# Optimization experiments

Hardware: AMD Instinct MI355X
Metric: run time of the kernel (lower is better)

The kernel has to match this reference:

```python
import jax, jax.numpy as jnp
import numpy as np

N_NODES = 50000
N_EDGES = 640000
F_IN = 64
EDGE_DIM = 16
HID = 128
N_LAYERS = 3
N_CLASSES = 2
NUM_GRAPHS = 64
BN_EPS = 1e-5


def setup_inputs() -> dict:
    key = jax.random.key(0)
    ks = jax.random.split(key, 20)
    s = 0.05
    inp = {
        "x": jax.random.normal(ks[0], (N_NODES, F_IN), dtype=jnp.float32),
        "edge_index": jax.random.randint(ks[1], (2, N_EDGES), 0, N_NODES, dtype=jnp.int32),
        "edge_attr": jax.random.normal(ks[2], (N_EDGES, EDGE_DIM), dtype=jnp.float32),
        "batch": jnp.sort(jax.random.randint(ks[3], (N_NODES,), 0, NUM_GRAPHS, dtype=jnp.int32)),
        # node encoder
        "enc_W": jax.random.normal(ks[4], (F_IN, HID), dtype=jnp.float32) * s,
        "enc_b": jnp.zeros((HID,), dtype=jnp.float32),
        # per-layer GINEConv params (stacked over layers)
        "edge_W": jax.random.normal(ks[5], (N_LAYERS, EDGE_DIM, HID), dtype=jnp.float32) * s,
        "edge_b": jnp.zeros((N_LAYERS, HID), dtype=jnp.float32),
        "mlp_W1": jax.random.normal(ks[6], (N_LAYERS, HID, HID), dtype=jnp.float32) * s,
        "mlp_b1": jnp.zeros((N_LAYERS, HID), dtype=jnp.float32),
        "mlp_W2": jax.random.normal(ks[7], (N_LAYERS, HID, HID), dtype=jnp.float32) * s,
        "mlp_b2": jnp.zeros((N_LAYERS, HID), dtype=jnp.float32),
        "bn_gamma": jnp.ones((N_LAYERS, HID), dtype=jnp.float32),
        "bn_beta": jnp.zeros((N_LAYERS, HID), dtype=jnp.float32),
        # classification head
        "head_W1": jax.random.normal(ks[8], (HID, HID), dtype=jnp.float32) * s,
        "head_b1": jnp.zeros((HID,), dtype=jnp.float32),
        "head_W2": jax.random.normal(ks[9], (HID, N_CLASSES), dtype=jnp.float32) * s,
        "head_b2": jnp.zeros((N_CLASSES,), dtype=jnp.float32),
    }
    return inp


def reference(x, edge_index, edge_attr, batch, enc_W, enc_b, edge_W, edge_b,
              mlp_W1, mlp_b1, mlp_W2, mlp_b2, bn_gamma, bn_beta,
              head_W1, head_b1, head_W2, head_b2):
    src, dst = edge_index[0], edge_index[1]  # message flows src -> dst
    h = x @ enc_W + enc_b  # [N, HID]
    for l in range(N_LAYERS):
        # GINEConv: msg = ReLU(x_src + Lin(edge_attr)); aggr = scatter_add at dst
        e = edge_attr @ edge_W[l] + edge_b[l]          # [E, HID]
        msg = jax.nn.relu(h[src] + e)                  # [E, HID]
        agg = jax.ops.segment_sum(msg, dst, num_segments=N_NODES)
        z = h + agg  # (1 + eps) * x + aggr, eps = 0
        # node MLP: Linear-ReLU-Linear
        z = jax.nn.relu(z @ mlp_W1[l] + mlp_b1[l]) @ mlp_W2[l] + mlp_b2[l]
        # BatchNorm1d (training-mode batch stats) + ReLU (dropout = identity)
        mean = jnp.mean(z, axis=0)
        var = jnp.var(z, axis=0)
        z = bn_gamma[l] * (z - mean) * jax.lax.rsqrt(var + BN_EPS) + bn_beta[l]
        h = jax.nn.relu(z)
    # global_add_pool over graphs
    g = jax.ops.segment_sum(h, batch, num_segments=NUM_GRAPHS)  # [G, HID]
    out = jax.nn.relu(g @ head_W1 + head_b1) @ head_W2 + head_b2
    return out  # [G, N_CLASSES]
```

## Files before the change

kernel.cpp:

```cpp
#include <hip/hip_runtime.h>
#include <hip/hip_bf16.h>

#define N_NODES 50000
#define N_EDGES 640000
#define F_IN 64
#define EDGE_DIM 16
#define HID 128
#define N_LAYERS 3
#define NUM_GRAPHS 64
#define BN_EPS 1e-5f

typedef __attribute__((ext_vector_type(8))) short short8;
typedef __attribute__((ext_vector_type(4))) float f32x4;
typedef __attribute__((ext_vector_type(2))) __fp16 half2v;

__device__ __forceinline__ float bfl(unsigned int u) {
    unsigned int v = u << 16; float f; __builtin_memcpy(&f, &v, 4); return f;
}
__device__ __forceinline__ float bfh(unsigned int u) {
    unsigned int v = u & 0xffff0000u; float f; __builtin_memcpy(&f, &v, 4); return f;
}
__device__ __forceinline__ unsigned int f2bf(float f) {
    unsigned int v; __builtin_memcpy(&v, &f, 4);
    v += 0x7fffu + ((v >> 16) & 1u);
    return v >> 16;
}
__device__ __forceinline__ unsigned int pack2(float lo, float hi) {
    return f2bf(lo) | (f2bf(hi) << 16);
}
__device__ __forceinline__ half2v u2h(unsigned int u) {
    half2v h; __builtin_memcpy(&h, &u, 4); return h;
}
__device__ __forceinline__ unsigned int pkh(float a, float b) {
    half2v h = __builtin_amdgcn_cvt_pkrtz(a, b);
    unsigned int u; __builtin_memcpy(&u, &h, 4); return u;
}

__global__ void k_hist(const int* __restrict__ dst, int* __restrict__ deg) {
    int e = blockIdx.x * 256 + threadIdx.x;
    atomicAdd(&deg[dst[e]], 1);
}

__global__ void k_blockred(const int* __restrict__ deg, int* __restrict__ bsums) {
    __shared__ int s[256];
    int i = blockIdx.x * 256 + threadIdx.x;
    int v = (i < N_NODES) ? deg[i] : 0;
    s[threadIdx.x] = v;
    __syncthreads();
    for (int off = 128; off > 0; off >>= 1) {
        if (threadIdx.x < off) s[threadIdx.x] += s[threadIdx.x + off];
        __syncthreads();
    }
    if (threadIdx.x == 0) bsums[blockIdx.x] = s[0];
}

__global__ void k_scan_bsums(int* __restrict__ bsums, int nb) {
    __shared__ int s[256];
    const int tid = threadIdx.x;
    const int v = (tid < nb) ? bsums[tid] : 0;
    s[tid] = v;
    __syncthreads();
    for (int off = 1; off < 256; off <<= 1) {
        int t = 0;
        if (tid >= off) t = s[tid - off];
        __syncthreads();
        s[tid] += t;
        __syncthreads();
    }
    if (tid < nb) bsums[tid] = s[tid] - v;
}

__global__ void k_scan_blocks(int* __restrict__ deg_rowptr, const int* __restrict__ bsums,
                              int* __restrict__ cursor) {
    __shared__ int s[256];
    int tid = threadIdx.x;
    int i = blockIdx.x * 256 + tid;
    int v = (i < N_NODES) ? deg_rowptr[i] : 0;
    s[tid] = v;
    __syncthreads();
    for (int off = 1; off < 256; off <<= 1) {
        int t = 0;
        if (tid >= off) t = s[tid - off];
        __syncthreads();
        s[tid] += t;
        __syncthreads();
    }
    int excl = s[tid] - v + bsums[blockIdx.x];
    if (i < N_NODES) {
        deg_rowptr[i] = excl;
        cursor[i] = excl;
    }
    if (i == N_NODES - 1) deg_rowptr[N_NODES] = N_EDGES;
}

__global__ void k_fill(const int* __restrict__ dst, int* __restrict__ cursor,
                       int* __restrict__ elist) {
    int e = blockIdx.x * 256 + threadIdx.x;
    int p = atomicAdd(&cursor[dst[e]], 1);
    elist[p] = e;
}

__global__ __launch_bounds__(256) void k_gather(const int* __restrict__ elist,
                                                const int* __restrict__ esrc,
                                                const float* __restrict__ eattr,
                                                int* __restrict__ src_s,
                                                uint4* __restrict__ eattr_h) {
    const int base = blockIdx.x * 1024;
    const int tid = threadIdx.x;
    int p[4], eid[4];
#pragma unroll
    for (int j = 0; j < 4; ++j) p[j] = base + tid + j * 256;
#pragma unroll
    for (int j = 0; j < 4; ++j) eid[j] = elist[p[j]];
    int sv[4];
#pragma unroll
    for (int j = 0; j < 4; ++j) sv[j] = esrc[eid[j]];
    float4 a[4][4];
#pragma unroll
    for (int j = 0; j < 4; ++j) {
        const float* ep = eattr + (size_t)eid[j] * EDGE_DIM;
        a[j][0] = *(const float4*)ep;
        a[j][1] = *(const float4*)(ep + 4);
        a[j][2] = *(const float4*)(ep + 8);
        a[j][3] = *(const float4*)(ep + 12);
    }
#pragma unroll
    for (int j = 0; j < 4; ++j) {
        src_s[p[j]] = sv[j];
        eattr_h[p[j] * 2] = make_uint4(pkh(a[j][0].x, a[j][0].y), pkh(a[j][0].z, a[j][0].w),
                                       pkh(a[j][1].x, a[j][1].y), pkh(a[j][1].z, a[j][1].w));
        eattr_h[p[j] * 2 + 1] = make_uint4(pkh(a[j][2].x, a[j][2].y), pkh(a[j][2].z, a[j][2].w),
                                           pkh(a[j][3].x, a[j][3].y), pkh(a[j][3].z, a[j][3].w));
    }
}

__global__ void k_pack(const float* __restrict__ W1, const float* __restrict__ W2,
                       const float* __restrict__ encW, const float* __restrict__ eW,
                       unsigned short* __restrict__ wp, unsigned short* __restrict__ wpe,
                       unsigned int* __restrict__ wek) {
    const int t = blockIdx.x * 256 + threadIdx.x;
    if (t < 12288) {
        const int mat = t >> 11;
        const int r = t & 2047;
        const int kstep = r >> 9;
        const int ntile = (r >> 6) & 7;
        const int lane = r & 63;
        const float* W = (mat < 3) ? (W1 + mat * 16384) : (W2 + (mat - 3) * 16384);
        const int kbase = kstep * 32 + ((lane >> 4) << 3);
        const int n = ntile * 16 + (lane & 15);
        unsigned int o[4];
#pragma unroll
        for (int jj = 0; jj < 4; ++jj)
            o[jj] = pack2(W[(kbase + 2 * jj) * HID + n], W[(kbase + 2 * jj + 1) * HID + n]);
        *(uint4*)(wp + (size_t)mat * 16384 + (((kstep << 3) + ntile) * 64 + lane) * 8) =
            make_uint4(o[0], o[1], o[2], o[3]);
    } else if (t < 13312) {
        const int r = t - 12288;
        const int kstep = r >> 9;
        const int ntile = (r >> 6) & 7;
        const int lane = r & 63;
        const int kbase = kstep * 32 + ((lane >> 4) << 3);
        const int n = ntile * 16 + (lane & 15);
        unsigned int o[4];
#pragma unroll
        for (int jj = 0; jj < 4; ++jj)
            o[jj] = pack2(encW[(kbase + 2 * jj) * HID + n], encW[(kbase + 2 * jj + 1) * HID + n]);
        *(uint4*)(wpe + (((kstep << 3) + ntile) * 64 + lane) * 8) =
            make_uint4(o[0], o[1], o[2], o[3]);
    } else {
        const int r = t - 13312;
        const int l = r >> 10;
        const int rr = r & 1023;
        const int kp = rr >> 7, f = rr & 127;
        const float a = eW[(l * EDGE_DIM + 2 * kp) * HID + f];
        const float b = eW[(l * EDGE_DIM + 2 * kp + 1) * HID + f];
        wek[r] = pkh(a, b);
    }
}

__global__ __launch_bounds__(256, 3) void k_encm(const float* __restrict__ x,
                                                 const unsigned short* __restrict__ wpe,
                                                 const float* __restrict__ b,
                                                 unsigned short* __restrict__ hb) {
    const int tid = threadIdx.x;
    const int w = tid >> 6, lane = tid & 63;
    const int q = lane >> 4, l15 = lane & 15;
    const int row0 = blockIdx.x * 64 + w * 16;
    const int ar = min(row0 + l15, N_NODES - 1);
    const float* xp = x + (size_t)ar * F_IN + q * 8;
    f32x4 acc[8];
#pragma unroll
    for (int nt = 0; nt < 8; ++nt) acc[nt] = (f32x4){0.f, 0.f, 0.f, 0.f};
#pragma unroll
    for (int ks = 0; ks < 2; ++ks) {
        const float4 v0 = *(const float4*)(xp + ks * 32);
        const float4 v1 = *(const float4*)(xp + ks * 32 + 4);
        unsigned int u[4] = {pack2(v0.x, v0.y), pack2(v0.z, v0.w),
                             pack2(v1.x, v1.y), pack2(v1.z, v1.w)};
        short8 a; __builtin_memcpy(&a, u, 16);
#pragma unroll
        for (int nt = 0; nt < 8; ++nt) {
            const short8 bf = *(const short8*)(wpe + (((ks << 3) + nt) * 64 + lane) * 8);
            acc[nt] = __builtin_amdgcn_mfma_f32_16x16x32_bf16(a, bf, acc[nt], 0, 0, 0);
        }
    }
    const int rowb = row0 + q * 4;
#pragma unroll
    for (int nt = 0; nt < 8; ++nt) {
        const float bias = b[nt * 16 + l15];
        const int cc = nt * 16 + l15;
#pragma unroll
        for (int reg = 0; reg < 4; ++reg) {
            const int r = rowb + reg;
            if (r < N_NODES)
                hb[(size_t)r * HID + cc] = (unsigned short)f2bf(acc[nt][reg] + bias);
        }
    }
}

__global__ __launch_bounds__(256, 2) void k_agg(const unsigned int* __restrict__ in32,
                                                const int* __restrict__ src_s,
                                                const uint4* __restrict__ eattr_h,
                                                const unsigned int* __restrict__ wek,
                                                const float* __restrict__ be,
                                                const int* __restrict__ row_ptr,
                                                const float* __restrict__ bnst,
                                                const float* __restrict__ gamma,
                                                const float* __restrict__ beta,
                                                const int bnmode,
                                                unsigned int* __restrict__ zb32) {
    const int lane = threadIdx.x & 63;
    const int wv = threadIdx.x >> 6;
    const int f2 = lane * 2;
    half2v wx[8], wy[8];
#pragma unroll
    for (int j = 0; j < 8; ++j) {
        wx[j] = u2h(wek[j * 128 + f2]);
        wy[j] = u2h(wek[j * 128 + f2 + 1]);
    }
    const float2 eb = *(const float2*)&be[f2];

    float2 sc = make_float2(1.f, 1.f), sh = make_float2(0.f, 0.f);
    float rlo = -3.4e38f;
    if (bnmode) {
        const float invN = 1.0f / (float)N_NODES;
        const float m0 = bnst[f2] * invN, m1 = bnst[f2 + 1] * invN;
        const float v0 = fmaxf(bnst[128 + f2] * invN - m0 * m0, 0.f);
        const float v1 = fmaxf(bnst[128 + f2 + 1] * invN - m1 * m1, 0.f);
        const float r0 = rsqrtf(v0 + BN_EPS), r1 = rsqrtf(v1 + BN_EPS);
        sc = make_float2(gamma[f2] * r0, gamma[f2 + 1] * r1);
        sh = make_float2(fmaf(-m0, sc.x, beta[f2]), fmaf(-m1, sc.y, beta[f2 + 1]));
        rlo = 0.f;
    }

    const int n = blockIdx.x * 4 + wv;
    const int base = __builtin_amdgcn_readfirstlane(row_ptr[n]);
    const int deg = __builtin_amdgcn_readfirstlane(row_ptr[n + 1]) - base;

    const unsigned int uself = in32[n * 64 + lane];
    float2 acc = make_float2(fmaxf(fmaf(bfl(uself), sc.x, sh.x), rlo),
                             fmaxf(fmaf(bfh(uself), sc.y, sh.y), rlo));

    if (deg > 0) {
        const int* sp = src_s + base;
        const uint4* ep = eattr_h + (size_t)base * 2;
        const int last = deg - 1;
        const int nch = (deg + 3) >> 2;

        unsigned int huC[4], huN[4];
        uint4 eaC[4][2], eaN[4][2];
        int s2[4];
        {
            int s0[4], s1[4];
#pragma unroll
            for (int j = 0; j < 4; ++j) s0[j] = sp[min(j, last)];
#pragma unroll
            for (int j = 0; j < 4; ++j) huC[j] = in32[s0[j] * 64 + lane];
#pragma unroll
            for (int j = 0; j < 4; ++j) s1[j] = sp[min(4 + j, last)];
            if (nch > 1) {
#pragma unroll
                for (int j = 0; j < 4; ++j) huN[j] = in32[s1[j] * 64 + lane];
            } else {
#pragma unroll
                for (int j = 0; j < 4; ++j) huN[j] = 0u;
            }
#pragma unroll
            for (int j = 0; j < 4; ++j) {
                const int e = min(j, last);
                eaC[j][0] = ep[e * 2]; eaC[j][1] = ep[e * 2 + 1];
            }
#pragma unroll
            for (int j = 0; j < 4; ++j) s2[j] = sp[min(8 + j, last)];
        }
        for (int c = 0; c < nch; ++c) {
            unsigned int huNN[4] = {0u, 0u, 0u, 0u};
            if (c + 2 < nch) {
#pragma unroll
                for (int j = 0; j < 4; ++j) huNN[j] = in32[s2[j] * 64 + lane];
            }
            int s3[4];
#pragma unroll
            for (int j = 0; j < 4; ++j) s3[j] = sp[min((c + 3) * 4 + j, last)];
            if (c + 1 < nch) {
#pragma unroll
                for (int j = 0; j < 4; ++j) {
                    const int e = min((c + 1) * 4 + j, last);
                    eaN[j][0] = ep[e * 2]; eaN[j][1] = ep[e * 2 + 1];
                }
            }
            __builtin_amdgcn_sched_barrier(0);
            const int rem = deg - c * 4;
#pragma unroll
            for (int j = 0; j < 4; ++j) {
                if (j < rem) {
                    const unsigned int* au = (const unsigned int*)&eaC[j][0];
                    float ex = eb.x, ey = eb.y;
#pragma unroll
                    for (int k = 0; k < 8; ++k) {
                        const half2v a = u2h(au[k]);
                        ex = __builtin_amdgcn_fdot2(a, wx[k], ex, false);
                        ey = __builtin_amdgcn_fdot2(a, wy[k], ey, false);
                    }
                    const float hx = fmaxf(fmaf(bfl(huC[j]), sc.x, sh.x), rlo);
                    const float hy = fmaxf(fmaf(bfh(huC[j]), sc.y, sh.y), rlo);
                    acc.x += fmaxf(hx + ex, 0.f);
                    acc.y += fmaxf(hy + ey, 0.f);
                }
            }
            if (c + 1 < nch) {
#pragma unroll
                for (int j = 0; j < 4; ++j) {
                    huC[j] = huN[j]; huN[j] = huNN[j];
                    eaC[j][0] = eaN[j][0]; eaC[j][1] = eaN[j][1];
                    s2[j] = s3[j];
                }
            }
        }
    }
    zb32[n * 64 + lane] = pack2(acc.x, acc.y);
}

#define Z1LD 136

__global__ __launch_bounds__(256, 3) void k_mlp(const unsigned short* __restrict__ zb,
                                                const unsigned short* __restrict__ w1p,
                                                const float* __restrict__ b1,
                                                const unsigned short* __restrict__ w2p,
                                                const float* __restrict__ b2,
                                                unsigned short* __restrict__ z2b,
                                                float* __restrict__ bn) {
    __shared__ unsigned short z1s[64 * Z1LD];
    __shared__ float redA[512];
    __shared__ float redB[512];
    const int tid = threadIdx.x;
    const int w = tid >> 6, lane = tid & 63;
    const int q = lane >> 4, l15 = lane & 15;
    const int row0 = blockIdx.x * 64 + w * 16;

    const int ar = min(row0 + l15, N_NODES - 1);
    const unsigned short* aptr = zb + (size_t)ar * HID + q * 8;

    f32x4 acc[8];
#pragma unroll
    for (int nt = 0; nt < 8; ++nt) acc[nt] = (f32x4){0.f, 0.f, 0.f, 0.f};

#pragma unroll
    for (int ks = 0; ks < 4; ++ks) {
        const short8 a = *(const short8*)(aptr + ks * 32);
#pragma unroll
        for (int nt = 0; nt < 8; ++nt) {
            const short8 b = *(const short8*)(w1p + (((ks << 3) + nt) * 64 + lane) * 8);
            acc[nt] = __builtin_amdgcn_mfma_f32_16x16x32_bf16(a, b, acc[nt], 0, 0, 0);
        }
    }
    {
        const int lr0 = w * 16 + q * 4;
#pragma unroll
        for (int nt = 0; nt < 8; ++nt) {
            const float bias = b1[nt * 16 + l15];
            const int cc = nt * 16 + l15;
#pragma unroll
            for (int reg = 0; reg < 4; ++reg) {
                const float v = fmaxf(acc[nt][reg] + bias, 0.f);
                z1s[(lr0 + reg) * Z1LD + cc] = (unsigned short)f2bf(v);
            }
        }
    }
#pragma unroll
    for (int nt = 0; nt < 8; ++nt) acc[nt] = (f32x4){0.f, 0.f, 0.f, 0.f};
    const unsigned short* a2p = &z1s[(w * 16 + l15) * Z1LD + q * 8];
#pragma unroll
    for (int ks = 0; ks < 4; ++ks) {
        const short8 a = *(const short8*)(a2p + ks * 32);
#pragma unroll
        for (int nt = 0; nt < 8; ++nt) {
            const short8 b = *(const short8*)(w2p + (((ks << 3) + nt) * 64 + lane) * 8);
            acc[nt] = __builtin_amdgcn_mfma_f32_16x16x32_bf16(a, b, acc[nt], 0, 0, 0);
        }
    }
    float s[8], sq[8];
    const int rowb = row0 + q * 4;
#pragma unroll
    for (int nt = 0; nt < 8; ++nt) {
        const float bias = b2[nt * 16 + l15];
        const int cc = nt * 16 + l15;
        float ls = 0.f, lq = 0.f;
#pragma unroll
        for (int reg = 0; reg < 4; ++reg) {
            const int r = rowb + reg;
            const float v = acc[nt][reg] + bias;
            if (r < N_NODES) {
                z2b[(size_t)r * HID + cc] = (unsigned short)f2bf(v);
                ls += v;
                lq = fmaf(v, v, lq);
            }
        }
        s[nt] = ls; sq[nt] = lq;
    }
#pragma unroll
    for (int nt = 0; nt < 8; ++nt) {
        s[nt] += __shfl_xor(s[nt], 16, 64);
        s[nt] += __shfl_xor(s[nt], 32, 64);
        sq[nt] += __shfl_xor(sq[nt], 16, 64);
        sq[nt] += __shfl_xor(sq[nt], 32, 64);
    }
    if (lane < 16) {
#pragma unroll
        for (int nt = 0; nt < 8; ++nt) {
            redA[w * 128 + nt * 16 + lane] = s[nt];
            redB[w * 128 + nt * 16 + lane] = sq[nt];
        }
    }
    __syncthreads();
    if (tid < 128) {
        float t = redA[tid] + redA[128 + tid] + redA[256 + tid] + redA[384 + tid];
        atomicAdd(&bn[tid], t);
    } else {
        const int c = tid - 128;
        float t = redB[c] + redB[128 + c] + redB[256 + c] + redB[384 + c];
        atomicAdd(&bn[128 + c], t);
    }
}

__global__ void k_pool(const unsigned short* __restrict__ z2b, const int* __restrict__ batch,
                       const float* __restrict__ bnst, const float* __restrict__ gamma,
                       const float* __restrict__ beta, float* __restrict__ g) {
    const int f = threadIdx.x;
    const float invN = 1.0f / (float)N_NODES;
    const float m = bnst[f] * invN;
    const float var = fmaxf(bnst[128 + f] * invN - m * m, 0.f);
    const float r = rsqrtf(var + BN_EPS);
    const float sc = gamma[f] * r;
    const float sh = fmaf(-m, sc, beta[f]);

    const int n0 = blockIdx.x * 128;
    const int nend = min(n0 + 128, N_NODES);
    float acc = 0.f;
    int cur = batch[n0];
    for (int n = n0; n < nend; ++n) {
        const int bb = batch[n];
        if (bb != cur) {
            atomicAdd(&g[cur * HID + f], acc);
            acc = 0.f;
            cur = bb;
        }
        const float raw = bfl((unsigned int)z2b[n * HID + f]);
        acc += fmaxf(fmaf(raw, sc, sh), 0.f);
    }
    atomicAdd(&g[cur * HID + f], acc);
}

__global__ void k_head1(const float* __restrict__ g, const float* __restrict__ W,
                        const float* __restrict__ b, float* __restrict__ g1) {
    const int idx = blockIdx.x * 256 + threadIdx.x;
    const int r = idx >> 7, c = idx & 127;
    float acc = b[c];
    for (int k = 0; k < 128; ++k) acc = fmaf(g[r * HID + k], W[k * HID + c], acc);
    g1[idx] = fmaxf(acc, 0.f);
}

__global__ void k_head2(const float* __restrict__ g1, const float* __restrict__ W,
                        const float* __restrict__ b, float* __restrict__ out) {
    const int idx = threadIdx.x;
    const int r = idx >> 1, c = idx & 1;
    float acc = b[c];
    for (int k = 0; k < 128; ++k) acc = fmaf(g1[r * HID + k], W[k * 2 + c], acc);
    out[idx] = acc;
}

extern "C" void kernel_launch(void* const* d_in, const int* in_sizes, int n_in,
                              void* d_out, int out_size, void* d_ws, size_t ws_size,
                              hipStream_t stream) {
    const float* x     = (const float*)d_in[0];
    const int*   ei    = (const int*)d_in[1];
    const float* eattr = (const float*)d_in[2];
    const int*   batch = (const int*)d_in[3];
    const float* encW  = (const float*)d_in[4];
    const float* encb  = (const float*)d_in[5];
    const float* eW    = (const float*)d_in[6];
    const float* eb    = (const float*)d_in[7];
    const float* W1    = (const float*)d_in[8];
    const float* b1    = (const float*)d_in[9];
    const float* W2    = (const float*)d_in[10];
    const float* b2    = (const float*)d_in[11];
    const float* gam   = (const float*)d_in[12];
    const float* bet   = (const float*)d_in[13];
    const float* hW1   = (const float*)d_in[14];
    const float* hb1   = (const float*)d_in[15];
    const float* hW2   = (const float*)d_in[16];
    const float* hb2   = (const float*)d_in[17];
    float* out = (float*)d_out;

    float* ws = (float*)d_ws;
    unsigned short* z2b = (unsigned short*)ws;
    float* bn  = ws + 3200000;
    float* g   = ws + 3200256;
    float* g1  = ws + 3208448;
    unsigned short* hb = (unsigned short*)(ws + 3216640);
    unsigned int* zb32 = (unsigned int*)(ws + 6416640);
    int* row_ptr = (int*)(ws + 11216640);
    int* cursor  = row_ptr + N_NODES + 1;
    int* elist   = cursor + N_NODES;
    int* bsums   = elist + N_EDGES;
    int* src_s   = bsums + 256;
    uint4* eattr_h = (uint4*)(ws + 12596900);
    unsigned short* wp  = (unsigned short*)(ws + 17716900);
    unsigned short* wpe = (unsigned short*)(ws + 17766100);
    unsigned int*   wek = (unsigned int*)(ws + 17770200);

    const int* esrc = ei;
    const int* edst = ei + N_EDGES;

    hipMemsetAsync(row_ptr, 0, (N_NODES + 1) * sizeof(int), stream);
    k_hist<<<N_EDGES / 256, 256, 0, stream>>>(edst, row_ptr);
    k_blockred<<<196, 256, 0, stream>>>(row_ptr, bsums);
    k_scan_bsums<<<1, 256, 0, stream>>>(bsums, 196);
    k_scan_blocks<<<196, 256, 0, stream>>>(row_ptr, bsums, cursor);
    k_fill<<<N_EDGES / 256, 256, 0, stream>>>(edst, cursor, elist);
    k_gather<<<N_EDGES / 1024, 256, 0, stream>>>(elist, esrc, eattr, src_s, eattr_h);

    k_pack<<<64, 256, 0, stream>>>(W1, W2, encW, eW, wp, wpe, wek);

    k_encm<<<782, 256, 0, stream>>>(x, wpe, encb, hb);

    for (int l = 0; l < N_LAYERS; ++l) {
        const unsigned int* in32 = (l == 0) ? (const unsigned int*)hb
                                            : (const unsigned int*)z2b;
        k_agg<<<12500, 256, 0, stream>>>(in32, src_s, eattr_h,
                                         wek + l * 1024, eb + l * HID, row_ptr,
                                         bn, gam + (l ? (l - 1) * HID : 0),
                                         bet + (l ? (l - 1) * HID : 0),
                                         (l > 0) ? 1 : 0, zb32);
        hipMemsetAsync(bn, 0, 256 * sizeof(float), stream);
        k_mlp<<<782, 256, 0, stream>>>((const unsigned short*)zb32,
                                       wp + (size_t)l * 16384, b1 + l * HID,
                                       wp + (size_t)(3 + l) * 16384, b2 + l * HID,
                                       z2b, bn);
    }

    hipMemsetAsync(g, 0, NUM_GRAPHS * HID * sizeof(float), stream);
    k_pool<<<391, 128, 0, stream>>>(z2b, batch, bn, gam + 2 * HID, bet + 2 * HID, g);
    k_head1<<<32, 256, 0, stream>>>(g, hW1, hb1, g1);
    k_head2<<<1, 128, 0, stream>>>(g1, hW2, hb2, out);
}
```

Baseline: 576.4 us.

## Compute edge linear via fp16 MFMA in aggregation, batching 16 edges per tile

```diff
diff --git a/kernel.cpp b/kernel.cpp
--- a/kernel.cpp
+++ b/kernel.cpp
@@ -13,6 +13,7 @@
 typedef __attribute__((ext_vector_type(8))) short short8;
 typedef __attribute__((ext_vector_type(4))) float f32x4;
 typedef __attribute__((ext_vector_type(2))) __fp16 half2v;
+typedef __attribute__((ext_vector_type(8))) __fp16 half8;
 
 __device__ __forceinline__ float bfl(unsigned int u) {
     unsigned int v = u << 16; float f; __builtin_memcpy(&f, &v, 4); return f;
@@ -27,9 +28,6 @@
 }
 __device__ __forceinline__ unsigned int pack2(float lo, float hi) {
     return f2bf(lo) | (f2bf(hi) << 16);
-}
-__device__ __forceinline__ half2v u2h(unsigned int u) {
-    half2v h; __builtin_memcpy(&h, &u, 4); return h;
 }
 __device__ __forceinline__ unsigned int pkh(float a, float b) {
     half2v h = __builtin_amdgcn_cvt_pkrtz(a, b);
@@ -136,8 +134,9 @@
 
 __global__ void k_pack(const float* __restrict__ W1, const float* __restrict__ W2,
                        const float* __restrict__ encW, const float* __restrict__ eW,
+                       const float* __restrict__ eb2,
                        unsigned short* __restrict__ wp, unsigned short* __restrict__ wpe,
-                       unsigned int* __restrict__ wek) {
+                       unsigned short* __restrict__ wekf) {
     const int t = blockIdx.x * 256 + threadIdx.x;
     if (t < 12288) {
         const int mat = t >> 11;
@@ -171,10 +170,20 @@
         const int r = t - 13312;
         const int l = r >> 10;
         const int rr = r & 1023;
-        const int kp = rr >> 7, f = rr & 127;
-        const float a = eW[(l * EDGE_DIM + 2 * kp) * HID + f];
-        const float b = eW[(l * EDGE_DIM + 2 * kp + 1) * HID + f];
-        wek[r] = pkh(a, b);
+        const int nt = rr >> 7;
+        const int lane = (rr >> 1) & 63;
+        const int hf = rr & 1;
+        const int qq = lane >> 4;
+        const int f = ((lane & 15) << 3) + nt;
+        float v[4];
+#pragma unroll
+        for (int j = 0; j < 4; ++j) {
+            const int k = (qq << 3) + (hf << 2) + j;
+            v[j] = (k < 16) ? eW[(l * EDGE_DIM + k) * HID + f]
+                            : ((k == 16) ? eb2[l * HID + f] : 0.f);
+        }
+        *(uint2*)(wekf + (((l * 8 + nt) * 64 + lane) * 8) + (hf << 2)) =
+            make_uint2(pkh(v[0], v[1]), pkh(v[2], v[3]));
     }
 }
 
@@ -218,11 +227,10 @@
     }
 }
 
-__global__ __launch_bounds__(256, 2) void k_agg(const unsigned int* __restrict__ in32,
+__global__ __launch_bounds__(256, 2) void k_agg(const unsigned short* __restrict__ hrow,
                                                 const int* __restrict__ src_s,
                                                 const uint4* __restrict__ eattr_h,
-                                                const unsigned int* __restrict__ wek,
-                                                const float* __restrict__ be,
+                                                const unsigned short* __restrict__ wekf,
                                                 const int* __restrict__ row_ptr,
                                                 const float* __restrict__ bnst,
                                                 const float* __restrict__ gamma,
@@ -231,114 +239,108 @@
                                                 unsigned int* __restrict__ zb32) {
     const int lane = threadIdx.x & 63;
     const int wv = threadIdx.x >> 6;
-    const int f2 = lane * 2;
-    half2v wx[8], wy[8];
-#pragma unroll
-    for (int j = 0; j < 8; ++j) {
-        wx[j] = u2h(wek[j * 128 + f2]);
-        wy[j] = u2h(wek[j * 128 + f2 + 1]);
-    }
-    const float2 eb = *(const float2*)&be[f2];
-
-    float2 sc = make_float2(1.f, 1.f), sh = make_float2(0.f, 0.f);
+    const int q = lane >> 4, l15 = lane & 15;
+    const int f0 = l15 * 8;
+
+    half8 Bf[8];
+#pragma unroll
+    for (int nt = 0; nt < 8; ++nt) {
+        uint4 u = *(const uint4*)(wekf + (nt * 64 + lane) * 8);
+        __builtin_memcpy(&Bf[nt], &u, 16);
+    }
+
+    float sc[8], sh[8];
     float rlo = -3.4e38f;
     if (bnmode) {
+        rlo = 0.f;
         const float invN = 1.0f / (float)N_NODES;
-        const float m0 = bnst[f2] * invN, m1 = bnst[f2 + 1] * invN;
-        const float v0 = fmaxf(bnst[128 + f2] * invN - m0 * m0, 0.f);
-        const float v1 = fmaxf(bnst[128 + f2 + 1] * invN - m1 * m1, 0.f);
-        const float r0 = rsqrtf(v0 + BN_EPS), r1 = rsqrtf(v1 + BN_EPS);
-        sc = make_float2(gamma[f2] * r0, gamma[f2 + 1] * r1);
-        sh = make_float2(fmaf(-m0, sc.x, beta[f2]), fmaf(-m1, sc.y, beta[f2 + 1]));
-        rlo = 0.f;
-    }
-
-    const int n = blockIdx.x * 4 + wv;
-    const int base = __builtin_amdgcn_readfirstlane(row_ptr[n]);
-    const int deg = __builtin_amdgcn_readfirstlane(row_ptr[n + 1]) - base;
-
-    const unsigned int uself = in32[n * 64 + lane];
-    float2 acc = make_float2(fmaxf(fmaf(bfl(uself), sc.x, sh.x), rlo),
-                             fmaxf(fmaf(bfh(uself), sc.y, sh.y), rlo));
-
-    if (deg > 0) {
-        const int* sp = src_s + base;
-        const uint4* ep = eattr_h + (size_t)base * 2;
-        const int last = deg - 1;
-        const int nch = (deg + 3) >> 2;
-
-        unsigned int huC[4], huN[4];
-        uint4 eaC[4][2], eaN[4][2];
-        int s2[4];
-        {
-            int s0[4], s1[4];
-#pragma unroll
-            for (int j = 0; j < 4; ++j) s0[j] = sp[min(j, last)];
-#pragma unroll
-            for (int j = 0; j < 4; ++j) huC[j] = in32[s0[j] * 64 + lane];
-#pragma unroll
-            for (int j = 0; j < 4; ++j) s1[j] = sp[min(4 + j, last)];
-            if (nch > 1) {
-#pragma unroll
-                for (int j = 0; j < 4; ++j) huN[j] = in32[s1[j] * 64 + lane];
-            } else {
-#pragma unroll
-                for (int j = 0; j < 4; ++j) huN[j] = 0u;
+#pragma unroll
+        for (int j = 0; j < 8; ++j) {
+            const int f = f0 + j;
+            const float m = bnst[f] * invN;
+            const float v = fmaxf(bnst[128 + f] * invN - m * m, 0.f);
+            const float r = rsqrtf(v + BN_EPS);
+            sc[j] = gamma[f] * r;
+            sh[j] = fmaf(-m, sc[j], beta[f]);
+        }
+    } else {
+#pragma unroll
+        for (int j = 0; j < 8; ++j) { sc[j] = 1.f; sh[j] = 0.f; }
+    }
+
+    const int wid = blockIdx.x * 4 + wv;
+    const int n0 = wid * 5;
+
+    for (int i = 0; i < 5; ++i) {
+        const int n = n0 + i;
+        const int base = __builtin_amdgcn_readfirstlane(row_ptr[n]);
+        const int deg  = __builtin_amdgcn_readfirstlane(row_ptr[n + 1]) - base;
+
+        float accf[8];
+#pragma unroll
+        for (int j = 0; j < 8; ++j) accf[j] = 0.f;
+
+        const int ntile = (deg + 15) >> 4;
+        for (int t = 0; t < ntile; ++t) {
+            const int e0 = t * 16;
+            uint4 au = make_uint4(0u, 0u, 0u, 0u);
+            if (q < 2) {
+                const int ea = min(e0 + l15, deg - 1);
+                au = eattr_h[(size_t)(base + ea) * 2 + q];
+            } else if (q == 2) {
+                au.x = 0x3C00u;
             }
-#pragma unroll
-            for (int j = 0; j < 4; ++j) {
-                const int e = min(j, last);
-                eaC[j][0] = ep[e * 2]; eaC[j][1] = ep[e * 2 + 1];
+            half8 Af; __builtin_memcpy(&Af, &au, 16);
+
+            int sv[4];
+#pragma unroll
+            for (int r = 0; r < 4; ++r)
+                sv[r] = src_s[base + min(e0 + q * 4 + r, deg - 1)];
+            uint4 hg[4];
+#pragma unroll
+            for (int r = 0; r < 4; ++r)
+                hg[r] = *(const uint4*)(hrow + (size_t)sv[r] * HID + f0);
+
+            f32x4 acc[8];
+#pragma unroll
+            for (int nt = 0; nt < 8; ++nt) {
+                acc[nt] = (f32x4){0.f, 0.f, 0.f, 0.f};
+                acc[nt] = __builtin_amdgcn_mfma_f32_16x16x32_f16(Af, Bf[nt], acc[nt], 0, 0, 0);
             }
-#pragma unroll
-            for (int j = 0; j < 4; ++j) s2[j] = sp[min(8 + j, last)];
-        }
-        for (int c = 0; c < nch; ++c) {
-            unsigned int huNN[4] = {0u, 0u, 0u, 0u};
-            if (c + 2 < nch) {
-#pragma unroll
-                for (int j = 0; j < 4; ++j) huNN[j] = in32[s2[j] * 64 + lane];
-            }
-            int s3[4];
-#pragma unroll
-            for (int j = 0; j < 4; ++j) s3[j] = sp[min((c + 3) * 4 + j, last)];
-            if (c + 1 < nch) {
-#pragma unroll
-                for (int j = 0; j < 4; ++j) {
-                    const int e = min((c + 1) * 4 + j, last);
-                    eaN[j][0] = ep[e * 2]; eaN[j][1] = ep[e * 2 + 1];
+
+#pragma unroll
+            for (int r = 0; r < 4; ++r) {
+                const float m = (e0 + q * 4 + r < deg) ? 1.f : 0.f;
+                const unsigned int* hu = (const unsigned int*)&hg[r];
+#pragma unroll
+                for (int p = 0; p < 4; ++p) {
+                    const float hA = fmaxf(fmaf(bfl(hu[p]), sc[2 * p],     sh[2 * p]),     rlo);
+                    const float hB = fmaxf(fmaf(bfh(hu[p]), sc[2 * p + 1], sh[2 * p + 1]), rlo);
+                    accf[2 * p]     = fmaf(m, fmaxf(hA + acc[2 * p][r],     0.f), accf[2 * p]);
+                    accf[2 * p + 1] = fmaf(m, fmaxf(hB + acc[2 * p + 1][r], 0.f), accf[2 * p + 1]);
                 }
             }
-            __builtin_amdgcn_sched_barrier(0);
-            const int rem = deg - c * 4;
-#pragma unroll
-            for (int j = 0; j < 4; ++j) {
-                if (j < rem) {
-                    const unsigned int* au = (const unsigned int*)&eaC[j][0];
-                    float ex = eb.x, ey = eb.y;
-#pragma unroll
-                    for (int k = 0; k < 8; ++k) {
-                        const half2v a = u2h(au[k]);
-                        ex = __builtin_amdgcn_fdot2(a, wx[k], ex, false);
-                        ey = __builtin_amdgcn_fdot2(a, wy[k], ey, false);
-                    }
-                    const float hx = fmaxf(fmaf(bfl(huC[j]), sc.x, sh.x), rlo);
-                    const float hy = fmaxf(fmaf(bfh(huC[j]), sc.y, sh.y), rlo);
-                    acc.x += fmaxf(hx + ex, 0.f);
-                    acc.y += fmaxf(hy + ey, 0.f);
-                }
+        }
+
+#pragma unroll
+        for (int j = 0; j < 8; ++j) {
+            accf[j] += __shfl_xor(accf[j], 16, 64);
+            accf[j] += __shfl_xor(accf[j], 32, 64);
+        }
+
+        if (q == 0) {
+            const uint4 hs = *(const uint4*)(hrow + (size_t)n * HID + f0);
+            const unsigned int* hu = (const unsigned int*)&hs;
+            unsigned int o[4];
+#pragma unroll
+            for (int p = 0; p < 4; ++p) {
+                const float hA = fmaxf(fmaf(bfl(hu[p]), sc[2 * p],     sh[2 * p]),     rlo);
+                const float hB = fmaxf(fmaf(bfh(hu[p]), sc[2 * p + 1], sh[2 * p + 1]), rlo);
+                o[p] = pack2(hA + accf[2 * p], hB + accf[2 * p + 1]);
             }
-            if (c + 1 < nch) {
-#pragma unroll
-                for (int j = 0; j < 4; ++j) {
-                    huC[j] = huN[j]; huN[j] = huNN[j];
-                    eaC[j][0] = eaN[j][0]; eaC[j][1] = eaN[j][1];
-                    s2[j] = s3[j];
-                }
-            }
-        }
-    }
-    zb32[n * 64 + lane] = pack2(acc.x, acc.y);
+            *(uint4*)(zb32 + (size_t)n * 64 + l15 * 4) = make_uint4(o[0], o[1], o[2], o[3]);
+        }
+    }
 }
 
 #define Z1LD 136
@@ -519,6 +521,7 @@
     float* g1  = ws + 3208448;
     unsigned short* hb = (unsigned short*)(ws + 3216640);
     unsigned int* zb32 = (unsigned int*)(ws + 6416640);
+    unsigned short* wekf = (unsigned short*)(ws + 9616640);
     int* row_ptr = (int*)(ws + 11216640);
     int* cursor  = row_ptr + N_NODES + 1;
     int* elist   = cursor + N_NODES;
@@ -527,7 +530,6 @@
     uint4* eattr_h = (uint4*)(ws + 12596900);
     unsigned short* wp  = (unsigned short*)(ws + 17716900);
     unsigned short* wpe = (unsigned short*)(ws + 17766100);
-    unsigned int*   wek = (unsigned int*)(ws + 17770200);
 
     const int* esrc = ei;
     const int* edst = ei + N_EDGES;
@@ -540,18 +542,17 @@
     k_fill<<<N_EDGES / 256, 256, 0, stream>>>(edst, cursor, elist);
     k_gather<<<N_EDGES / 1024, 256, 0, stream>>>(elist, esrc, eattr, src_s, eattr_h);
 
-    k_pack<<<64, 256, 0, stream>>>(W1, W2, encW, eW, wp, wpe, wek);
+    k_pack<<<64, 256, 0, stream>>>(W1, W2, encW, eW, eb, wp, wpe, wekf);
 
     k_encm<<<782, 256, 0, stream>>>(x, wpe, encb, hb);
 
     for (int l = 0; l < N_LAYERS; ++l) {
-        const unsigned int* in32 = (l == 0) ? (const unsigned int*)hb
-                                            : (const unsigned int*)z2b;
-        k_agg<<<12500, 256, 0, stream>>>(in32, src_s, eattr_h,
-                                         wek + l * 1024, eb + l * HID, row_ptr,
-                                         bn, gam + (l ? (l - 1) * HID : 0),
-                                         bet + (l ? (l - 1) * HID : 0),
-                                         (l > 0) ? 1 : 0, zb32);
+        const unsigned short* hrow = (l == 0) ? hb : z2b;
+        k_agg<<<2500, 256, 0, stream>>>(hrow, src_s, eattr_h,
+                                        wekf + (size_t)l * 4096, row_ptr,
+                                        bn, gam + (l ? (l - 1) * HID : 0),
+                                        bet + (l ? (l - 1) * HID : 0),
+                                        (l > 0) ? 1 : 0, zb32);
         hipMemsetAsync(bn, 0, 256 * sizeof(float), stream);
         k_mlp<<<782, 256, 0, stream>>>((const unsigned short*)zb32,
                                        wp + (size_t)l * 16384, b1 + l * HID,
```

Result: faster. 538.4 us (-6.6%).
